# Kernel tuning notes

Hardware: AMD Instinct MI355X
Metric: run time of the kernel (lower is better)

The kernel has to match this reference:

```python
import jax, jax.numpy as jnp
import numpy as np

N = 20000      # nodes
E = 200000     # edges
F_IN = 512     # num_features
H = 1024       # hidden (hard-coded in module)
OUT = 128      # output_size


def setup_inputs() -> dict:
    key = jax.random.key(0)
    ks = jax.random.split(key, 12)
    x = jax.random.normal(ks[0], (N, F_IN), jnp.float32)
    edge_index = jax.random.randint(ks[1], (2, E), 0, N, dtype=jnp.int32)
    edge_weight = jax.random.uniform(ks[2], (E,), jnp.float32)
    # GCNConv weights (glorot-ish) and biases
    w1 = jax.random.normal(ks[3], (F_IN, H), jnp.float32) / np.sqrt(F_IN)
    b1 = jnp.zeros((H,), jnp.float32)
    w2 = jax.random.normal(ks[4], (H, OUT), jnp.float32) / np.sqrt(H)
    b2 = jnp.zeros((OUT,), jnp.float32)
    # residual Linear layers
    rw1 = jax.random.normal(ks[5], (F_IN, H), jnp.float32) / np.sqrt(F_IN)
    rb1 = jax.random.normal(ks[6], (H,), jnp.float32) * 0.01
    rw2 = jax.random.normal(ks[7], (H, OUT), jnp.float32) / np.sqrt(H)
    rb2 = jax.random.normal(ks[8], (OUT,), jnp.float32) * 0.01
    return {"x": x, "w1": w1, "b1": b1, "w2": w2, "b2": b2,
            "rw1": rw1, "rb1": rb1, "rw2": rw2, "rb2": rb2,
            "edge_weight": edge_weight, "edge_index": edge_index}


def gcn_conv(x, W, b, edge_index, edge_weight, n):
    """PyG GCNConv: linear transform, add self-loops (weight 1), sym-normalized scatter-add."""
    xw = x @ W                                             # [n, d_out]
    loop = jnp.arange(n, dtype=edge_index.dtype)
    row = jnp.concatenate([edge_index[0], loop])           # sources (x_j)
    col = jnp.concatenate([edge_index[1], loop])           # targets (aggregate here)
    ew = jnp.concatenate([edge_weight, jnp.ones((n,), xw.dtype)])
    deg = jax.ops.segment_sum(ew, col, num_segments=n)     # weighted in-degree
    dis = jnp.where(deg > 0, jax.lax.rsqrt(jnp.where(deg > 0, deg, 1.0)), 0.0)
    norm = dis[row] * ew * dis[col]                        # [E+n]
    msg = xw[row] * norm[:, None]                          # gather + scale
    out = jax.ops.segment_sum(msg, col, num_segments=n)    # scatter-add
    return out + b


def reference(x, w1, b1, w2, b2, rw1, rb1, rw2, rb2, edge_weight, edge_index):
    n = x.shape[0]
    h = jax.nn.relu(gcn_conv(x, w1, b1, edge_index, edge_weight, n) + (x @ rw1 + rb1))
    # F.dropout(training=False) is identity in eval mode
    out = gcn_conv(h, w2, b2, edge_index, edge_weight, n) + (h @ rw2 + rb2)
    return out
```

## Files before the change

kernel.cpp:

```cpp
#include <hip/hip_runtime.h>
#include <hip/hip_bf16.h>

#define NN 20000
#define EE 200000
#define FIN 512
#define HID 1024
#define OUTF 128
#define MPAD 20224

typedef unsigned short ush;
typedef __attribute__((ext_vector_type(8))) short bf16x8;
typedef __attribute__((ext_vector_type(4))) float f32x4;

__device__ __forceinline__ ush f2bf_rne(float f) {
    union { float f; unsigned u; } a; a.f = f;
    unsigned u = a.u;
    return (ush)((u + 0x7fffu + ((u >> 16) & 1u)) >> 16);
}
__device__ __forceinline__ float bf2f(ush h) {
    union { float f; unsigned u; } a; a.u = ((unsigned)h) << 16;
    return a.f;
}
__device__ __forceinline__ void split_bf(float v, ush& hi, ush& lo) {
    hi = f2bf_rne(v);
    lo = f2bf_rne(v - bf2f(hi));
}

__device__ __forceinline__ void gl16(const void* g, void* l) {
    __builtin_amdgcn_global_load_lds(
        (const __attribute__((address_space(1))) unsigned*)g,
        (__attribute__((address_space(3))) unsigned*)l, 16, 0, 0);
}

__global__ void init_kernel(float* deg, int* cnt, int n,
                            const float* __restrict__ b1, const float* __restrict__ rb1,
                            const float* __restrict__ b2, const float* __restrict__ rb2,
                            float* bias1s, float* bias2c) {
    int i = blockIdx.x * blockDim.x + threadIdx.x;
    if (i < n) { deg[i] = 1.0f; cnt[i] = 0; }
    if (i < HID) bias1s[i] = b1[i] + rb1[i];
    if (i < 256) bias2c[i] = (i < 128) ? 0.0f : (b2[i - 128] + rb2[i - 128]);
}

__global__ void deg_count_kernel(const int* __restrict__ ei, const float* __restrict__ ew,
                                 float* deg, int* cnt, int e) {
    int idx = blockIdx.x * blockDim.x + threadIdx.x;
    if (idx < e) {
        int c = ei[EE + idx];
        atomicAdd(&deg[c], ew[idx]);
        atomicAdd(&cnt[c], 1);
    }
}

#define SCAN_THREADS 1024
#define SCAN_CHUNK 20
__global__ __launch_bounds__(SCAN_THREADS)
void scan_kernel(const int* __restrict__ cnt, int* rowptr, int* cursor, int n, int total_e,
                 const float* __restrict__ deg, float* __restrict__ dis) {
    __shared__ int part[SCAN_THREADS];
    int t = threadIdx.x;
    int base = t * SCAN_CHUNK;
    int s = 0;
    for (int j = 0; j < SCAN_CHUNK; ++j) {
        int i = base + j;
        if (i < n) { s += cnt[i]; dis[i] = rsqrtf(deg[i]); }
    }
    part[t] = s;
    __syncthreads();
    for (int off = 1; off < SCAN_THREADS; off <<= 1) {
        int add = (t >= off) ? part[t - off] : 0;
        __syncthreads();
        part[t] += add;
        __syncthreads();
    }
    int run = (t == 0) ? 0 : part[t - 1];
    for (int j = 0; j < SCAN_CHUNK; ++j) {
        int i = base + j;
        if (i < n) { rowptr[i] = run; cursor[i] = run; run += cnt[i]; }
    }
    if (t == SCAN_THREADS - 1) rowptr[n] = total_e;
}

__global__ void scatter_kernel(const int* __restrict__ ei, const float* __restrict__ ew,
                               const float* __restrict__ dis, int* cursor,
                               int* srcs, float* norms, int e) {
    int idx = blockIdx.x * blockDim.x + threadIdx.x;
    if (idx < e) {
        int r = ei[idx];
        int c = ei[EE + idx];
        float nv = dis[r] * ew[idx] * dis[c];
        int p = atomicAdd(&cursor[c], 1);
        srcs[p] = r;
        norms[p] = nv;
    }
}

__global__ __launch_bounds__(256)
void tsplit_kernel(const float* __restrict__ src, int K, int N,
                   ush* __restrict__ dh, ush* __restrict__ dl, int ldst, int koff) {
    __shared__ float tile[32][33];
    int tx = threadIdx.x & 31, ty = threadIdx.x >> 5;
    int n0 = blockIdx.x * 32, k0 = blockIdx.y * 32;
#pragma unroll
    for (int i = 0; i < 4; ++i)
        tile[ty * 4 + i][tx] = src[(size_t)(k0 + ty * 4 + i) * N + n0 + tx];
    __syncthreads();
#pragma unroll
    for (int i = 0; i < 4; ++i) {
        int n = n0 + ty * 4 + i, k = k0 + tx;
        float v = tile[tx][ty * 4 + i];
        ush h, lo; split_bf(v, h, lo);
        size_t off = (size_t)n * ldst + koff + k;
        dh[off] = h;
        dl[off] = lo;
    }
}

__global__ __launch_bounds__(128)
void aggx_kernel(const float* __restrict__ x,
                 ush* __restrict__ xh, ush* __restrict__ xl,
                 ush* __restrict__ axh, ush* __restrict__ axl,
                 const float* __restrict__ dis,
                 const int* __restrict__ rowptr, const int* __restrict__ srcs,
                 const float* __restrict__ norms) {
    int i = blockIdx.x;
    int t = threadIdx.x;
    float d = dis[i];
    float d2 = d * d;
    float4 v = ((const float4*)(x + (size_t)i * FIN))[t];

    ushort4 vh, vl;
    split_bf(v.x, vh.x, vl.x); split_bf(v.y, vh.y, vl.y);
    split_bf(v.z, vh.z, vl.z); split_bf(v.w, vh.w, vl.w);
    ((ushort4*)(xh + (size_t)i * FIN))[t] = vh;
    ((ushort4*)(xl + (size_t)i * FIN))[t] = vl;

    float s0 = d2 * v.x, s1 = d2 * v.y, s2 = d2 * v.z, s3 = d2 * v.w;
    int beg = rowptr[i], end = rowptr[i + 1];
    int j = beg;
    for (; j + 2 <= end; j += 2) {
        int sa = srcs[j], sb = srcs[j + 1];
        float wa = norms[j], wb = norms[j + 1];
        float4 ua = ((const float4*)(x + (size_t)sa * FIN))[t];
        float4 ub = ((const float4*)(x + (size_t)sb * FIN))[t];
        s0 += wa * ua.x + wb * ub.x;
        s1 += wa * ua.y + wb * ub.y;
        s2 += wa * ua.z + wb * ub.z;
        s3 += wa * ua.w + wb * ub.w;
    }
    if (j < end) {
        int sa = srcs[j];
        float wa = norms[j];
        float4 ua = ((const float4*)(x + (size_t)sa * FIN))[t];
        s0 += wa * ua.x; s1 += wa * ua.y; s2 += wa * ua.z; s3 += wa * ua.w;
    }
    ushort4 hv, lv;
    split_bf(s0, hv.x, lv.x); split_bf(s1, hv.y, lv.y);
    split_bf(s2, hv.z, lv.z); split_bf(s3, hv.w, lv.w);
    ((ushort4*)(axh + (size_t)i * FIN))[t] = hv;
    ((ushort4*)(axl + (size_t)i * FIN))[t] = lv;
}

__global__ __launch_bounds__(256)
void gemm_mfma(const ush* __restrict__ A0h, const ush* __restrict__ A0l,
               const ush* __restrict__ A1h, const ush* __restrict__ A1l,
               int ksw, int KA,
               const ush* __restrict__ BTh, const ush* __restrict__ BTl,
               const float* __restrict__ bias,
               float* __restrict__ Cf, ush* __restrict__ Chh, ush* __restrict__ Chl,
               int M, int N, int K, int mode) {
    __shared__ ush Ah[128 * 32], Al[128 * 32], Bh[128 * 32], Bl[128 * 32];

    int nwg = gridDim.x * gridDim.y;
    int orig = blockIdx.y * gridDim.x + blockIdx.x;
    int xcd = orig & 7, slot = orig >> 3;
    int q = nwg >> 3, r = nwg & 7;
    int wg = (xcd < r ? xcd * (q + 1) : r * (q + 1) + (xcd - r) * q) + slot;
    int bn = (wg % gridDim.x) * 128;
    int bm = (wg / gridDim.x) * 128;

    int t = threadIdx.x;
    int l = t & 63, w = t >> 6;
    int wr = w >> 1, wc = w & 1;

    int sr = t >> 2;
    int sg8 = (t & 3) * 8;
    size_t a_off0 = (size_t)(bm + sr) * KA + sg8;
    size_t a_off1 = (size_t)(bm + 64 + sr) * KA + sg8;
    size_t b_off0 = (size_t)(bn + sr) * K + sg8;
    size_t b_off1 = (size_t)(bn + 64 + sr) * K + sg8;
    int lo0 = t * 16, lo1 = t * 16 + 4096;

    int abase = (wr * 64 + (l & 15)) * 64 + ((l >> 4) << 4);
    int bbase = (wc * 64 + (l & 15)) * 64 + ((l >> 4) << 4);

    f32x4 acc[4][4];
#pragma unroll
    for (int i = 0; i < 4; ++i)
#pragma unroll
        for (int j = 0; j < 4; ++j) acc[i][j] = (f32x4){0.f, 0.f, 0.f, 0.f};

    for (int kt = 0; kt < K; kt += 32) {
        const ush* Asrch; const ush* Asrcl; int kk;
        if (kt < ksw) { Asrch = A0h; Asrcl = A0l; kk = kt; }
        else          { Asrch = A1h; Asrcl = A1l; kk = kt - ksw; }

        gl16(Asrch + a_off0 + kk, (char*)Ah + lo0);
        gl16(Asrch + a_off1 + kk, (char*)Ah + lo1);
        gl16(Asrcl + a_off0 + kk, (char*)Al + lo0);
        gl16(Asrcl + a_off1 + kk, (char*)Al + lo1);
        gl16(BTh + b_off0 + kt, (char*)Bh + lo0);
        gl16(BTh + b_off1 + kt, (char*)Bh + lo1);
        gl16(BTl + b_off0 + kt, (char*)Bl + lo0);
        gl16(BTl + b_off1 + kt, (char*)Bl + lo1);
        __syncthreads();

        bf16x8 ah[4], al[4], bh[4], bl[4];
#pragma unroll
        for (int f = 0; f < 4; ++f) {
            ah[f] = *(const bf16x8*)((const char*)Ah + abase + f * 1024);
            al[f] = *(const bf16x8*)((const char*)Al + abase + f * 1024);
            bh[f] = *(const bf16x8*)((const char*)Bh + bbase + f * 1024);
            bl[f] = *(const bf16x8*)((const char*)Bl + bbase + f * 1024);
        }
#pragma unroll
        for (int fm = 0; fm < 4; ++fm)
#pragma unroll
            for (int fn = 0; fn < 4; ++fn)
                acc[fm][fn] = __builtin_amdgcn_mfma_f32_16x16x32_bf16(ah[fm], bh[fn], acc[fm][fn], 0, 0, 0);
#pragma unroll
        for (int fm = 0; fm < 4; ++fm)
#pragma unroll
            for (int fn = 0; fn < 4; ++fn)
                acc[fm][fn] = __builtin_amdgcn_mfma_f32_16x16x32_bf16(ah[fm], bl[fn], acc[fm][fn], 0, 0, 0);
#pragma unroll
        for (int fm = 0; fm < 4; ++fm)
#pragma unroll
            for (int fn = 0; fn < 4; ++fn)
                acc[fm][fn] = __builtin_amdgcn_mfma_f32_16x16x32_bf16(al[fm], bh[fn], acc[fm][fn], 0, 0, 0);
        __syncthreads();
    }

    int ccol = bn + wc * 64 + (l & 15);
    float bb[4];
#pragma unroll
    for (int fn = 0; fn < 4; ++fn) bb[fn] = bias ? bias[ccol + fn * 16] : 0.0f;

    if (mode) {
#pragma unroll
        for (int fm = 0; fm < 4; ++fm)
#pragma unroll
            for (int j = 0; j < 4; ++j) {
                int row = bm + wr * 64 + fm * 16 + ((l >> 4) << 2) + j;
                if (row < M) {
#pragma unroll
                    for (int fn = 0; fn < 4; ++fn) {
                        float v = fmaxf(acc[fm][fn][j] + bb[fn], 0.0f);
                        ush hi, lo; split_bf(v, hi, lo);
                        size_t off = (size_t)row * N + ccol + fn * 16;
                        Chh[off] = hi;
                        Chl[off] = lo;
                    }
                }
            }
    } else {
#pragma unroll
        for (int fm = 0; fm < 4; ++fm)
#pragma unroll
            for (int j = 0; j < 4; ++j) {
                int row = bm + wr * 64 + fm * 16 + ((l >> 4) << 2) + j;
                if (row < M) {
#pragma unroll
                    for (int fn = 0; fn < 4; ++fn)
                        Cf[(size_t)row * N + ccol + fn * 16] = acc[fm][fn][j] + bb[fn];
                }
            }
    }
}

__global__ __launch_bounds__(256)
void agg2_kernel(const float* __restrict__ z2, const float* __restrict__ dis,
                 const int* __restrict__ rowptr, const int* __restrict__ srcs,
                 const float* __restrict__ norms, float* __restrict__ out) {
    int wave = threadIdx.x >> 6;
    int lane = threadIdx.x & 63;
    int i = blockIdx.x * 4 + wave;
    float d = dis[i];
    float d2 = d * d;
    float2 v = ((const float2*)(z2 + (size_t)i * 256))[lane];
    float ax = d2 * v.x, ay = d2 * v.y;
    int beg = rowptr[i], end = rowptr[i + 1];
    int j = beg;
    for (; j + 2 <= end; j += 2) {
        int sa = srcs[j], sb = srcs[j + 1];
        float wa = norms[j], wb = norms[j + 1];
        float2 ua = ((const float2*)(z2 + (size_t)sa * 256))[lane];
        float2 ub = ((const float2*)(z2 + (size_t)sb * 256))[lane];
        ax += wa * ua.x + wb * ub.x;
        ay += wa * ua.y + wb * ub.y;
    }
    if (j < end) {
        int sa = srcs[j];
        float wa = norms[j];
        float2 ua = ((const float2*)(z2 + (size_t)sa * 256))[lane];
        ax += wa * ua.x; ay += wa * ua.y;
    }
    float2 rr = ((const float2*)(z2 + (size_t)i * 256 + 128))[lane];
    float2 o; o.x = ax + rr.x; o.y = ay + rr.y;
    ((float2*)(out + (size_t)i * OUTF))[lane] = o;
}

extern "C" void kernel_launch(void* const* d_in, const int* in_sizes, int n_in,
                              void* d_out, int out_size, void* d_ws, size_t ws_size,
                              hipStream_t stream) {
    const float* x   = (const float*)d_in[0];
    const float* w1  = (const float*)d_in[1];
    const float* b1  = (const float*)d_in[2];
    const float* w2  = (const float*)d_in[3];
    const float* b2  = (const float*)d_in[4];
    const float* rw1 = (const float*)d_in[5];
    const float* rb1 = (const float*)d_in[6];
    const float* rw2 = (const float*)d_in[7];
    const float* rb2 = (const float*)d_in[8];
    const float* ew  = (const float*)d_in[9];
    const int*   ei  = (const int*)d_in[10];
    float* out = (float*)d_out;

    char* p = (char*)d_ws;
    ush* xh  = (ush*)p; p += (size_t)MPAD * FIN * 2;
    ush* xl  = (ush*)p; p += (size_t)MPAD * FIN * 2;
    ush* axh = (ush*)p; p += (size_t)MPAD * FIN * 2;
    ush* axl = (ush*)p; p += (size_t)MPAD * FIN * 2;
    ush* hh  = (ush*)p; p += (size_t)MPAD * HID * 2;
    ush* hl  = (ush*)p; p += (size_t)MPAD * HID * 2;
    ush* w1cth = (ush*)p; p += (size_t)HID * HID * 2;
    ush* w1ctl = (ush*)p; p += (size_t)HID * HID * 2;
    ush* w2cth = (ush*)p; p += (size_t)256 * HID * 2;
    ush* w2ctl = (ush*)p; p += (size_t)256 * HID * 2;
    float* deg    = (float*)p; p += NN * 4;
    float* dis    = (float*)p; p += NN * 4;
    float* norms  = (float*)p; p += EE * 4;
    float* bias1s = (float*)p; p += HID * 4;
    float* bias2c = (float*)p; p += 256 * 4;
    int* rowptr = (int*)p; p += (NN + 1) * 4;
    int* cursor = (int*)p; p += NN * 4;
    int* cnt    = (int*)p; p += NN * 4;
    int* srcs   = (int*)p; p += EE * 4;
    float* z2 = (float*)xh;

    init_kernel<<<(NN + 255) / 256, 256, 0, stream>>>(deg, cnt, NN, b1, rb1, b2, rb2, bias1s, bias2c);
    deg_count_kernel<<<(EE + 255) / 256, 256, 0, stream>>>(ei, ew, deg, cnt, EE);
    scan_kernel<<<1, SCAN_THREADS, 0, stream>>>(cnt, rowptr, cursor, NN, EE, deg, dis);
    scatter_kernel<<<(EE + 255) / 256, 256, 0, stream>>>(ei, ew, dis, cursor, srcs, norms, EE);

    { dim3 g(HID / 32, FIN / 32); tsplit_kernel<<<g, 256, 0, stream>>>(w1,  FIN, HID, w1cth, w1ctl, HID, 0);   }
    { dim3 g(HID / 32, FIN / 32); tsplit_kernel<<<g, 256, 0, stream>>>(rw1, FIN, HID, w1cth, w1ctl, HID, FIN); }
    { dim3 g(OUTF / 32, HID / 32); tsplit_kernel<<<g, 256, 0, stream>>>(w2,  HID, OUTF, w2cth, w2ctl, HID, 0); }
    { dim3 g(OUTF / 32, HID / 32); tsplit_kernel<<<g, 256, 0, stream>>>(rw2, HID, OUTF,
                                        w2cth + (size_t)128 * HID, w2ctl + (size_t)128 * HID, HID, 0); }

    aggx_kernel<<<NN, 128, 0, stream>>>(x, xh, xl, axh, axl, dis, rowptr, srcs, norms);

    {
        dim3 grid(HID / 128, MPAD / 128);
        gemm_mfma<<<grid, 256, 0, stream>>>(axh, axl, xh, xl, FIN, FIN,
                                            w1cth, w1ctl, bias1s,
                                            nullptr, hh, hl,
                                            NN, HID, HID, 1);
    }
    {
        dim3 grid(256 / 128, MPAD / 128);
        gemm_mfma<<<grid, 256, 0, stream>>>(hh, hl, hh, hl, HID, HID,
                                            w2cth, w2ctl, bias2c,
                                            z2, nullptr, nullptr,
                                            NN, 256, HID, 0);
    }
    agg2_kernel<<<NN / 4, 256, 0, stream>>>(z2, dis, rowptr, srcs, norms, out);
}
```

Baseline: 463.2 us.

## Add specialized triple-buffered MFMA GEMM for first layer with async global-to-LDS loads

Replaces the generic gemm_mfma call for the first layer with a dedicated kernel that hard-codes the split-bf16 (hi/lo) three-segment K loop over concatenated [AX|X] inputs. It uses a 3-stage LDS ring filled by direct global-to-LDS loads, with a partial vmcnt wait, so loads for tile k+2 overlap the MFMAs on tile k. It also adds swizzled LDS addressing, setprio around the MFMA block, and a fused bias+ReLU+bf16 split epilogue. The cost is more LDS per block and hand-placed waitcnt/barrier scheduling, which could be fragile.

After: 654.0 us. 41.2% more time.

```diff
diff --git a/kernel.cpp b/kernel.cpp
--- a/kernel.cpp
+++ b/kernel.cpp
@@ -159,6 +159,110 @@
     split_bf(s2, hv.z, lv.z); split_bf(s3, hv.w, lv.w);
     ((ushort4*)(axh + (size_t)i * FIN))[t] = hv;
     ((ushort4*)(axl + (size_t)i * FIN))[t] = lv;
+}
+
+__global__ __launch_bounds__(256, 4)
+void gemm_vk(const ush* __restrict__ axh, const ush* __restrict__ axl,
+             const ush* __restrict__ xh,  const ush* __restrict__ xl,
+             const ush* __restrict__ bth, const ush* __restrict__ btl,
+             const float* __restrict__ bias,
+             ush* __restrict__ Chh, ush* __restrict__ Chl) {
+    __shared__ ush LA[3][4096];
+    __shared__ ush LB[3][4096];
+
+    int nwg = gridDim.x * gridDim.y;
+    int orig = blockIdx.y * gridDim.x + blockIdx.x;
+    int xcd = orig & 7, slot0 = orig >> 3;
+    int q = nwg >> 3, r = nwg & 7;
+    int wg = (xcd < r ? xcd * (q + 1) : r * (q + 1) + (xcd - r) * q) + slot0;
+    int bn = (wg % gridDim.x) * 128;
+    int bm = (wg / gridDim.x) * 128;
+
+    int t = threadIdx.x;
+    int l = t & 63, w = t >> 6;
+    int wr = w >> 1, wc = w & 1;
+
+    int r0 = t >> 2;
+    int sc = (t & 3) ^ ((t >> 3) & 3);
+    int ld0 = t * 16, ld1 = t * 16 + 4096;
+
+    int xa = (l >> 4) ^ (((l & 15) >> 1) & 3);
+    int abase = (wr * 64 + (l & 15)) * 64 + xa * 16;
+    int bbase = (wc * 64 + (l & 15)) * 64 + xa * 16;
+
+    auto stage = [&](int kt, int s) {
+        int seg = kt >> 5;
+        int kk = (kt & 31) << 5;
+        const ush* Ap = (seg < 2) ? ((kk < FIN) ? axh : xh)
+                                  : ((kk < FIN) ? axl : xl);
+        int ka = kk & (FIN - 1);
+        const ush* Bp = (seg == 1) ? btl : bth;
+        gl16(Ap + (size_t)(bm + r0) * FIN + ka + sc * 8,       (char*)LA[s] + ld0);
+        gl16(Ap + (size_t)(bm + r0 + 64) * FIN + ka + sc * 8,  (char*)LA[s] + ld1);
+        gl16(Bp + (size_t)(bn + r0) * HID + kk + sc * 8,       (char*)LB[s] + ld0);
+        gl16(Bp + (size_t)(bn + r0 + 64) * HID + kk + sc * 8,  (char*)LB[s] + ld1);
+    };
+
+    f32x4 acc[4][4];
+#pragma unroll
+    for (int i = 0; i < 4; ++i)
+#pragma unroll
+        for (int j = 0; j < 4; ++j) acc[i][j] = (f32x4){0.f, 0.f, 0.f, 0.f};
+
+    stage(0, 0);
+    stage(1, 1);
+    asm volatile("s_waitcnt vmcnt(0)" ::: "memory");
+    __builtin_amdgcn_s_barrier();
+    __builtin_amdgcn_sched_barrier(0);
+
+    for (int kt = 0; kt < 96; ++kt) {
+        int s = kt % 3;
+        int s2 = (kt + 2) % 3;
+        int nx = (kt + 2 <= 95) ? kt + 2 : 95;
+        stage(nx, s2);
+
+        bf16x8 a[4], b[4];
+#pragma unroll
+        for (int fm = 0; fm < 4; ++fm)
+            a[fm] = *(const bf16x8*)((const char*)LA[s] + abase + fm * 1024);
+#pragma unroll
+        for (int fn = 0; fn < 4; ++fn)
+            b[fn] = *(const bf16x8*)((const char*)LB[s] + bbase + fn * 1024);
+
+        __builtin_amdgcn_s_setprio(1);
+#pragma unroll
+        for (int fm = 0; fm < 4; ++fm)
+#pragma unroll
+            for (int fn = 0; fn < 4; ++fn)
+                acc[fm][fn] = __builtin_amdgcn_mfma_f32_16x16x32_bf16(a[fm], b[fn], acc[fm][fn], 0, 0, 0);
+        __builtin_amdgcn_s_setprio(0);
+
+        __builtin_amdgcn_sched_barrier(0);
+        asm volatile("s_waitcnt vmcnt(4)" ::: "memory");
+        __builtin_amdgcn_s_barrier();
+        __builtin_amdgcn_sched_barrier(0);
+    }
+
+    int ccol = bn + wc * 64 + (l & 15);
+    float bb[4];
+#pragma unroll
+    for (int fn = 0; fn < 4; ++fn) bb[fn] = bias[ccol + fn * 16];
+#pragma unroll
+    for (int fm = 0; fm < 4; ++fm)
+#pragma unroll
+        for (int j = 0; j < 4; ++j) {
+            int row = bm + wr * 64 + fm * 16 + ((l >> 4) << 2) + j;
+            if (row < NN) {
+#pragma unroll
+                for (int fn = 0; fn < 4; ++fn) {
+                    float v = fmaxf(acc[fm][fn][j] + bb[fn], 0.0f);
+                    ush hi, lo; split_bf(v, hi, lo);
+                    size_t off = (size_t)row * HID + ccol + fn * 16;
+                    Chh[off] = hi;
+                    Chl[off] = lo;
+                }
+            }
+        }
 }
 
 __global__ __launch_bounds__(256)
@@ -363,10 +467,7 @@
 
     {
         dim3 grid(HID / 128, MPAD / 128);
-        gemm_mfma<<<grid, 256, 0, stream>>>(axh, axl, xh, xl, FIN, FIN,
-                                            w1cth, w1ctl, bias1s,
-                                            nullptr, hh, hl,
-                                            NN, HID, HID, 1);
+        gemm_vk<<<grid, 256, 0, stream>>>(axh, axl, xh, xl, w1cth, w1ctl, bias1s, hh, hl);
     }
     {
         dim3 grid(256 / 128, MPAD / 128);
```
